# Optimization experiments

Measured on AMD Instinct MI355X. Metric: run time of the kernel, lower is better.

The kernel has to match this reference:

```python
import jax, jax.numpy as jnp
import numpy as np

V = 778   # MANO mesh vertex count (hard-coded in the module)
K = 9     # spiral neighborhood length
C = 256   # in_channels
OUT = 3   # out_channels (per-vertex offset xyz)
B3 = 192  # 3 * B, B = 64


def setup_inputs() -> dict:
    key = jax.random.key(0)
    ks = jax.random.split(key, 12)
    x = jax.random.normal(ks[0], (B3, V, C), jnp.float32)
    pred_occ = jax.random.normal(ks[1], (B3, 2, 5), jnp.float32)
    indices = jax.random.randint(ks[2], (V, K), 0, V)
    finger_sizes = [112, 120, 124, 116, 108]
    fingers = {f"finger{i}": jax.random.randint(ks[3 + i], (n,), 0, V)
               for i, n in enumerate(finger_sizes)}

    def lin(k, fan_in, fan_out):
        kw, kb = jax.random.split(k)
        w = jax.random.normal(kw, (fan_in, fan_out), jnp.float32) / np.float32(np.sqrt(fan_in))
        b = jax.random.normal(kb, (fan_out,), jnp.float32) * 0.01
        return w, b

    w0, b0 = lin(ks[8], 2 * C * K, 2 * C)
    w1, b1 = lin(ks[9], 2 * C * K, C)
    w2, b2 = lin(ks[10], C * K, C)
    wh, bh = lin(ks[11], C * K, OUT)
    return {"x": x, "pred_occ": pred_occ, "indices": indices, **fingers,
            "w0": w0, "b0": b0, "w1": w1, "b1": b1, "w2": w2, "b2": b2,
            "wh": wh, "bh": bh}


def spiral_conv(x, idx, w, b):
    # x: [B, V, Cin], idx: [V, K] -> gather spiral neighbors, flatten, linear
    B = x.shape[0]
    g = x[:, idx.reshape(-1), :].reshape(B, V, -1)  # [B, V, K*Cin]
    return g @ w + b


def reference(x, pred_occ, indices, finger0, finger1, finger2, finger3, finger4,
              w0, b0, w1, b1, w2, b2, wh, bh):
    # Per-finger non-occlusion probabilities: softmax over class dim, take class 0
    occ = jax.nn.softmax(pred_occ, axis=1)[:, 0, :5]          # [3B, 5]
    weights = jnp.ones((x.shape[0], V), x.dtype)
    for i, fidx in enumerate([finger0, finger1, finger2, finger3, finger4]):
        val = jnp.broadcast_to(occ[:, i:i + 1], (x.shape[0], fidx.shape[0]))
        weights = weights.at[:, fidx].set(val)
    B = x.shape[0] // 3
    wv = jnp.stack(jnp.split(weights, 3, axis=0), axis=-1)[..., None]  # [B, V, 3, 1]
    wv = jax.nn.softmax(wv, axis=2)
    xv = jnp.stack(jnp.split(x, 3, axis=0), axis=2)                    # [B, V, 3, C]
    wx = jnp.sum(wv * xv, axis=2)                                      # [B, V, C]
    h = jnp.concatenate([wx, x[:B]], axis=2)                           # [B, V, 2C]
    h = jax.nn.relu(spiral_conv(h, indices, w0, b0))
    h = jax.nn.relu(spiral_conv(h, indices, w1, b1))
    h = jax.nn.relu(spiral_conv(h, indices, w2, b2))
    return spiral_conv(h, indices, wh, bh)                             # [B, V, 3]
```

## Files before the change

kernel.cpp:

```cpp
#include <hip/hip_runtime.h>

typedef unsigned short ushort_t;
typedef __attribute__((ext_vector_type(8))) __bf16 bf16x8;
typedef __attribute__((ext_vector_type(8))) unsigned short ushort8;
typedef __attribute__((ext_vector_type(4))) float floatx4;
typedef __attribute__((ext_vector_type(16))) float floatx16;

#define VN 778
#define KNB 9

__device__ __forceinline__ float bf2f(unsigned short s) {
  union { unsigned int u; float f; } x; x.u = ((unsigned int)s) << 16; return x.f;
}
__device__ __forceinline__ unsigned short f2bf(float f) {
  union { float f; unsigned int u; } x; x.f = f;
  unsigned int r = x.u + 0x7fffu + ((x.u >> 16) & 1u);
  return (unsigned short)(r >> 16);
}

__device__ __forceinline__ void load_lds16(const void* g, void* l) {
  __builtin_amdgcn_global_load_lds(
      (const __attribute__((address_space(1))) unsigned int*)g,
      (__attribute__((address_space(3))) unsigned int*)l, 16, 0, 0);
}

__global__ void prep_misc(const float* __restrict__ pred_occ,
                          const int* f0, const int* f1, const int* f2,
                          const int* f3, const int* f4,
                          int n0, int n1, int n2, int n3, int n4,
                          const float* __restrict__ wh,
                          float* __restrict__ occ, int* __restrict__ fid,
                          float* __restrict__ whT) {
  int t = threadIdx.x;
  for (int i = t; i < 192 * 5; i += 256) {
    int r = i / 5, f = i % 5;
    float p0 = pred_occ[r * 10 + f];
    float p1 = pred_occ[r * 10 + 5 + f];
    occ[i] = 1.0f / (1.0f + __expf(p1 - p0));
  }
  for (int i = t; i < VN; i += 256) fid[i] = -1;
  __syncthreads();
  const int* fp[5] = {f0, f1, f2, f3, f4};
  int fn[5] = {n0, n1, n2, n3, n4};
  for (int fi = 0; fi < 5; ++fi) {
    for (int i = t; i < fn[fi]; i += 256) fid[fp[fi][i]] = fi;
    __syncthreads();
  }
  for (int i = t; i < 3 * 2304; i += 256) {
    int o = i / 2304, k = i % 2304;
    whT[i] = wh[k * 3 + o];
  }
}

__global__ void wx_kernel(const float* __restrict__ x, const float* __restrict__ occ,
                          const int* __restrict__ fid, ushort_t* __restrict__ wx) {
  int g = blockIdx.x * 256 + threadIdx.x;
  int c8 = (g & 31) << 3;
  int bv = g >> 5;
  int b = bv / VN;
  int v = bv - b * VN;
  int f = fid[v];
  float w0 = 1.f, w1 = 1.f, w2 = 1.f;
  if (f >= 0) {
    w0 = occ[b * 5 + f];
    w1 = occ[(64 + b) * 5 + f];
    w2 = occ[(128 + b) * 5 + f];
  }
  float m = fmaxf(w0, fmaxf(w1, w2));
  float e0 = __expf(w0 - m), e1 = __expf(w1 - m), e2 = __expf(w2 - m);
  float inv = 1.0f / (e0 + e1 + e2);
  e0 *= inv; e1 *= inv; e2 *= inv;
  size_t base = (size_t)bv * 256 + c8;
  const size_t V1 = (size_t)64 * VN * 256, V2 = (size_t)128 * VN * 256;
  floatx4 x0a = *(const floatx4*)(x + base);
  floatx4 x0b = *(const floatx4*)(x + base + 4);
  floatx4 x1a = *(const floatx4*)(x + V1 + base);
  floatx4 x1b = *(const floatx4*)(x + V1 + base + 4);
  floatx4 x2a = *(const floatx4*)(x + V2 + base);
  floatx4 x2b = *(const floatx4*)(x + V2 + base + 4);
  ushort8 o;
#pragma unroll
  for (int e = 0; e < 4; ++e) {
    o[e]     = f2bf(e0 * x0a[e] + e1 * x1a[e] + e2 * x2a[e]);
    o[e + 4] = f2bf(e0 * x0b[e] + e1 * x1b[e] + e2 * x2b[e]);
  }
  *(ushort8*)(wx + base) = o;
}

__global__ void xcvt_kernel(const float* __restrict__ x, ushort_t* __restrict__ xb) {
  int g = blockIdx.x * 256 + threadIdx.x;
  size_t base = (size_t)g * 8;
  floatx4 fa = *(const floatx4*)(x + base);
  floatx4 fb = *(const floatx4*)(x + base + 4);
  ushort8 o;
#pragma unroll
  for (int e = 0; e < 4; ++e) { o[e] = f2bf(fa[e]); o[e + 4] = f2bf(fb[e]); }
  *(ushort8*)(xb + base) = o;
}

__global__ void pack_w(const float* __restrict__ w, ushort_t* __restrict__ wP,
                       int N, int ksn, int total) {
  int chunk = blockIdx.x * 256 + threadIdx.x;
  if (chunk >= total) return;
  int lane = chunk & 63;
  int rest = chunk >> 6;
  int ks = rest % ksn;
  int tn = rest / ksn;
  int n = (tn << 5) + (lane & 31);
  int kb = (ks << 4) + ((lane >> 5) << 3);
  ushort8 o;
#pragma unroll
  for (int j = 0; j < 8; ++j) o[j] = f2bf(w[(size_t)(kb + j) * N + n]);
  *(ushort8*)(wP + (size_t)chunk * 8) = o;
}

__global__ void pack_w64(const float* __restrict__ w, ushort_t* __restrict__ wP,
                         int N, int ksn, int total) {
  int chunk = blockIdx.x * 256 + threadIdx.x;
  if (chunk >= total) return;
  int lane = chunk & 63;
  int idx2 = chunk >> 6;
  int sub = idx2 & 1;
  int rest = idx2 >> 1;
  int ks = rest % ksn;
  int tn64 = rest / ksn;
  int n = (tn64 << 6) + (sub << 5) + (lane & 31);
  int kb = (ks << 4) + ((lane >> 5) << 3);
  ushort8 o;
#pragma unroll
  for (int j = 0; j < 8; ++j) o[j] = f2bf(w[(size_t)(kb + j) * N + n]);
  *(ushort8*)(wP + (size_t)chunk * 8) = o;
}

template <int CIN, int MODE, int WN>
__global__ __launch_bounds__(512, (WN == 64 ? 2 : 4)) void spiral_gemm(
    const ushort_t* __restrict__ act0, const float* __restrict__ actF,
    const ushort_t* __restrict__ actB, const ushort_t* __restrict__ wP,
    const float* __restrict__ bias, const int* __restrict__ idx,
    ushort_t* __restrict__ out, int NOUT) {
  constexpr int H = CIN / 128;
  constexpr int P = KNB * H;
  constexpr int KtotSteps = KNB * (CIN / 16);
  __shared__ __align__(16) ushort_t Alds[2][2048 * 8];
  const int v0 = blockIdx.x * 2;
  const int n0 = blockIdx.y << 8;
  const int tid = threadIdx.x;
  const int lane = tid & 63;
  const int wv = tid >> 6;
  const int mlo = lane & 31;
  const int q = lane >> 5;
  const int xm = mlo & 7;
  floatx16 c00{}, c01{}, c10{}, c11{}, c20{}, c21{}, c30{}, c31{};
  const ushort_t* bp;
  if constexpr (WN == 32) {
    const int tn0 = (n0 >> 5) + wv;
    bp = wP + (size_t)tn0 * KtotSteps * 512 + lane * 8;
  } else {
    bp = wP + (size_t)wv * KtotSteps * 1024 + lane * 8;
  }
  const int* iv0 = idx + v0 * KNB;
  const int* iv1 = iv0 + KNB;
  const int aoff0 = mlo * 128;
  const int aoff1 = (mlo + 32) * 128;
  const int aoff2 = 8192 + mlo * 128;
  const int aoff3 = 8192 + (mlo + 32) * 128;

  auto dma_stage = [&](int p, ushort_t* buf) {
    const int nbr = p / H, h = p - nbr * H;
    const int nva = iv0[nbr], nvb = iv1[nbr];
#pragma unroll
    for (int it = 0; it < 4; ++it) {
      const int slotb = ((wv << 2) + it) << 6;
      const int s = slotb + lane;
      const int vv = s >> 10;
      const int row = (s >> 4) & 63;
      const int ck = (s & 15) ^ (row & 7);
      const int nv = vv ? nvb : nva;
      const ushort_t* src;
      if (MODE == 0) {
        src = act0 + ((size_t)(row * VN + nv)) * CIN + h * 128 + ck * 8;
      } else {
        const ushort_t* basep = (MODE == 1 || h < 2) ? act0 : actB;
        src = basep + ((size_t)(row * VN + nv)) * 256 + (h & 1) * 128 + ck * 8;
      }
      load_lds16(src, buf + (size_t)slotb * 8);
    }
  };
  auto f32_stage = [&](int p, ushort_t* buf) {
    const int nbr = p / H, h = p - nbr * H;
    const int nva = iv0[nbr], nvb = iv1[nbr];
#pragma unroll
    for (int j = 0; j < 4; ++j) {
      const int s = (j << 9) + tid;
      const int vv = s >> 10;
      const int row = (s >> 4) & 63;
      const int ck = (s & 15) ^ (row & 7);
      const int nv = vv ? nvb : nva;
      const float* src = actF + ((size_t)(row * VN + nv)) * 256 + (h - 2) * 128 + ck * 8;
      floatx4 fa = *(const floatx4*)src;
      floatx4 fb = *(const floatx4*)(src + 4);
      ushort8 o;
#pragma unroll
      for (int e = 0; e < 4; ++e) { o[e] = f2bf(fa[e]); o[e + 4] = f2bf(fb[e]); }
      *(ushort8*)(buf + (size_t)s * 8) = o;
    }
  };

  dma_stage(0, Alds[0]);
  __syncthreads();
#pragma unroll 2
  for (int p = 0; p < P; ++p) {
    ushort_t* cur = Alds[p & 1];
    ushort_t* nxt = Alds[(p + 1) & 1];
    const bool have_next = (p + 1 < P);
    const bool next_f32 = (MODE == 1) && (((p + 1) & (H - 1)) >= 2);
    if (have_next && !next_f32) dma_stage(p + 1, nxt);
#pragma unroll
    for (int ks = 0; ks < 8; ++ks) {
      const int cko = ((((ks << 1) + q) ^ xm) << 3);
      if constexpr (WN == 32) {
        bf16x8 a0 = *(const bf16x8*)(cur + aoff0 + cko);
        bf16x8 a1 = *(const bf16x8*)(cur + aoff1 + cko);
        bf16x8 a2 = *(const bf16x8*)(cur + aoff2 + cko);
        bf16x8 a3 = *(const bf16x8*)(cur + aoff3 + cko);
        bf16x8 bv0 = *(const bf16x8*)bp; bp += 512;
        c00 = __builtin_amdgcn_mfma_f32_32x32x16_bf16(a0, bv0, c00, 0, 0, 0);
        c10 = __builtin_amdgcn_mfma_f32_32x32x16_bf16(a1, bv0, c10, 0, 0, 0);
        c20 = __builtin_amdgcn_mfma_f32_32x32x16_bf16(a2, bv0, c20, 0, 0, 0);
        c30 = __builtin_amdgcn_mfma_f32_32x32x16_bf16(a3, bv0, c30, 0, 0, 0);
      } else {
        bf16x8 a0 = *(const bf16x8*)(cur + aoff0 + cko);
        bf16x8 a1 = *(const bf16x8*)(cur + aoff1 + cko);
        bf16x8 a2 = *(const bf16x8*)(cur + aoff2 + cko);
        bf16x8 a3 = *(const bf16x8*)(cur + aoff3 + cko);
        bf16x8 b0 = *(const bf16x8*)bp;
        bf16x8 b1 = *(const bf16x8*)(bp + 512);
        bp += 1024;
        c00 = __builtin_amdgcn_mfma_f32_32x32x16_bf16(a0, b0, c00, 0, 0, 0);
        c10 = __builtin_amdgcn_mfma_f32_32x32x16_bf16(a1, b0, c10, 0, 0, 0);
        c20 = __builtin_amdgcn_mfma_f32_32x32x16_bf16(a2, b0, c20, 0, 0, 0);
        c30 = __builtin_amdgcn_mfma_f32_32x32x16_bf16(a3, b0, c30, 0, 0, 0);
        c01 = __builtin_amdgcn_mfma_f32_32x32x16_bf16(a0, b1, c01, 0, 0, 0);
        c11 = __builtin_amdgcn_mfma_f32_32x32x16_bf16(a1, b1, c11, 0, 0, 0);
        c21 = __builtin_amdgcn_mfma_f32_32x32x16_bf16(a2, b1, c21, 0, 0, 0);
        c31 = __builtin_amdgcn_mfma_f32_32x32x16_bf16(a3, b1, c31, 0, 0, 0);
      }
    }
    __syncthreads();
    if (have_next && next_f32) { f32_stage(p + 1, nxt); __syncthreads(); }
  }
  if constexpr (WN == 32) {
    const int n = n0 + (wv << 5) + mlo;
    const float bn = bias[n];
#pragma unroll
    for (int t = 0; t < 4; ++t) {
      const floatx16 av = (t == 0) ? c00 : (t == 1) ? c10 : (t == 2) ? c20 : c30;
      const int vcur = v0 + (t >> 1);
      const int bbase = (t & 1) << 5;
#pragma unroll
      for (int r = 0; r < 16; ++r) {
        const int m = (r & 3) + ((r >> 2) << 3) + (q << 2);
        float val = av[r] + bn; val = val > 0.f ? val : 0.f;
        out[((size_t)((bbase + m) * VN + vcur)) * NOUT + n] = f2bf(val);
      }
    }
  } else {
    const int nbase = (wv << 6) + mlo;
    const float bn0 = bias[nbase];
    const float bn1 = bias[nbase + 32];
#pragma unroll
    for (int t = 0; t < 8; ++t) {
      const int aj = t >> 1;
      const int ni = t & 1;
      const floatx16 av = (t == 0) ? c00 : (t == 1) ? c01 : (t == 2) ? c10 :
                          (t == 3) ? c11 : (t == 4) ? c20 : (t == 5) ? c21 :
                          (t == 6) ? c30 : c31;
      const int vcur = v0 + (aj >> 1);
      const int bbase = (aj & 1) << 5;
      const int n = nbase + (ni << 5);
      const float bn = ni ? bn1 : bn0;
#pragma unroll
      for (int r = 0; r < 16; ++r) {
        const int m = (r & 3) + ((r >> 2) << 3) + (q << 2);
        float val = av[r] + bn; val = val > 0.f ? val : 0.f;
        out[((size_t)((bbase + m) * VN + vcur)) * NOUT + n] = f2bf(val);
      }
    }
  }
}

__global__ void head_kernel(const ushort_t* __restrict__ act, const float* __restrict__ whT,
                            const float* __restrict__ bh, const int* __restrict__ idx,
                            float* __restrict__ out) {
  __shared__ __align__(16) ushort_t Alds[64 * 256];
  const int v = blockIdx.x;
  const int tid = threadIdx.x;
  float a0 = 0.f, a1 = 0.f, a2 = 0.f;
  const int b = tid;
  const int xm = b & 7;
  for (int nbr = 0; nbr < KNB; ++nbr) {
    const int nv = idx[v * KNB + nbr];
    __syncthreads();
#pragma unroll
    for (int it = 0; it < 8; ++it) {
      int L = it * 256 + tid;
      int bb = L >> 5;
      int jj = L & 31;
      ushort8 val = *(const ushort8*)(act + ((size_t)(bb * VN + nv)) * 256 + (jj << 3));
      int slot = jj ^ (bb & 7);
      *(ushort8*)&Alds[(size_t)(bb * 32 + slot) * 8] = val;
    }
    __syncthreads();
    if (tid < 64) {
      const float* wp = whT + nbr * 256;
#pragma unroll 4
      for (int j = 0; j < 32; ++j) {
        int jj = j ^ xm;
        ushort8 a8 = *(const ushort8*)&Alds[(b * 32 + jj) * 8];
#pragma unroll
        for (int e = 0; e < 8; ++e) {
          float av = bf2f(a8[e]);
          int k = (j << 3) + e;
          a0 += av * wp[k];
          a1 += av * wp[2304 + k];
          a2 += av * wp[4608 + k];
        }
      }
    }
  }
  if (tid < 64) {
    size_t o = ((size_t)(b * VN + v)) * 3;
    out[o + 0] = a0 + bh[0];
    out[o + 1] = a1 + bh[1];
    out[o + 2] = a2 + bh[2];
  }
}

extern "C" void kernel_launch(void* const* d_in, const int* in_sizes, int n_in,
                              void* d_out, int out_size, void* d_ws, size_t ws_size,
                              hipStream_t stream) {
  const float* x        = (const float*)d_in[0];
  const float* pred_occ = (const float*)d_in[1];
  const int* indices    = (const int*)d_in[2];
  const int* f0 = (const int*)d_in[3];
  const int* f1 = (const int*)d_in[4];
  const int* f2 = (const int*)d_in[5];
  const int* f3 = (const int*)d_in[6];
  const int* f4 = (const int*)d_in[7];
  const float* w0 = (const float*)d_in[8];
  const float* b0 = (const float*)d_in[9];
  const float* w1 = (const float*)d_in[10];
  const float* b1 = (const float*)d_in[11];
  const float* w2 = (const float*)d_in[12];
  const float* b2 = (const float*)d_in[13];
  const float* wh = (const float*)d_in[14];
  const float* bh = (const float*)d_in[15];
  float* outp = (float*)d_out;

  char* ws = (char*)d_ws;
  ushort_t* wP0 = (ushort_t*)(ws + 0);
  ushort_t* wP1 = (ushort_t*)(ws + 4718592);
  ushort_t* wP2 = (ushort_t*)(ws + 7077888);
  float* whT    = (float*)(ws + 8257536);
  float* occ    = (float*)(ws + 8285184);
  int* fid      = (int*)(ws + 8289024);
  ushort_t* R0  = (ushort_t*)(ws + 8292352);
  ushort_t* R1  = (ushort_t*)(ws + 33785856);
  ushort_t* XB  = (ushort_t*)(ws + 84772864);
  const bool useXB = (ws_size >= 110266368ull);

  prep_misc<<<1, 256, 0, stream>>>(pred_occ, f0, f1, f2, f3, f4,
                                   in_sizes[3], in_sizes[4], in_sizes[5],
                                   in_sizes[6], in_sizes[7], wh, occ, fid, whT);
  pack_w64<<<294912 / 256, 256, 0, stream>>>(w0, wP0, 512, 288, 294912);
  pack_w<<<147456 / 256, 256, 0, stream>>>(w1, wP1, 256, 288, 147456);
  pack_w<<<73728 / 256, 256, 0, stream>>>(w2, wP2, 256, 144, 73728);
  if (useXB) xcvt_kernel<<<6224, 256, 0, stream>>>(x, XB);
  wx_kernel<<<6224, 256, 0, stream>>>(x, occ, fid, R0);

  if (useXB)
    spiral_gemm<512, 2, 64><<<dim3(389, 1), 512, 0, stream>>>(R0, nullptr, XB, wP0, b0,
                                                              indices, R1, 512);
  else
    spiral_gemm<512, 1, 64><<<dim3(389, 1), 512, 0, stream>>>(R0, x, nullptr, wP0, b0,
                                                              indices, R1, 512);
  spiral_gemm<512, 0, 32><<<dim3(389, 1), 512, 0, stream>>>(R1, nullptr, nullptr, wP1, b1,
                                                            indices, R0, 256);
  spiral_gemm<256, 0, 32><<<dim3(389, 1), 512, 0, stream>>>(R0, nullptr, nullptr, wP2, b2,
                                                            indices, R1, 256);
  head_kernel<<<VN, 256, 0, stream>>>(R1, whT, bh, indices, outp);
  (void)n_in; (void)out_size;
}
```

Measured before the change: 825.0 us.

## Triple-buffer LDS gather pipeline in first spiral GEMM layer

Splits the wide first-layer spiral GEMM into its own kernel that keeps three LDS buffers and issues the gather DMA two stages ahead. It replaces the per-stage double-buffer __syncthreads with explicit vmcnt waits and a single barrier, and raises MFMA wave priority during compute. Neighbor indices are cached in shared memory once per block. The aim is to hide global-to-LDS gather latency behind MFMA work, at the cost of more LDS per block and fragile hand-written waitcnt ordering. The narrower layers keep the old double-buffered path.

```diff
diff --git a/kernel.cpp b/kernel.cpp
--- a/kernel.cpp
+++ b/kernel.cpp
@@ -132,8 +132,8 @@
   *(ushort8*)(wP + (size_t)chunk * 8) = o;
 }
 
-template <int CIN, int MODE, int WN>
-__global__ __launch_bounds__(512, (WN == 64 ? 2 : 4)) void spiral_gemm(
+template <int CIN, int MODE>
+__global__ __launch_bounds__(512, 2) void spiral_gemm_p(
     const ushort_t* __restrict__ act0, const float* __restrict__ actF,
     const ushort_t* __restrict__ actB, const ushort_t* __restrict__ wP,
     const float* __restrict__ bias, const int* __restrict__ idx,
@@ -141,9 +141,9 @@
   constexpr int H = CIN / 128;
   constexpr int P = KNB * H;
   constexpr int KtotSteps = KNB * (CIN / 16);
-  __shared__ __align__(16) ushort_t Alds[2][2048 * 8];
+  __shared__ __align__(16) ushort_t Alds[3][2048 * 8];
+  __shared__ int nbrsL[2 * KNB];
   const int v0 = blockIdx.x * 2;
-  const int n0 = blockIdx.y << 8;
   const int tid = threadIdx.x;
   const int lane = tid & 63;
   const int wv = tid >> 6;
@@ -151,23 +151,17 @@
   const int q = lane >> 5;
   const int xm = mlo & 7;
   floatx16 c00{}, c01{}, c10{}, c11{}, c20{}, c21{}, c30{}, c31{};
-  const ushort_t* bp;
-  if constexpr (WN == 32) {
-    const int tn0 = (n0 >> 5) + wv;
-    bp = wP + (size_t)tn0 * KtotSteps * 512 + lane * 8;
-  } else {
-    bp = wP + (size_t)wv * KtotSteps * 1024 + lane * 8;
-  }
-  const int* iv0 = idx + v0 * KNB;
-  const int* iv1 = iv0 + KNB;
+  const ushort_t* bp = wP + (size_t)wv * KtotSteps * 1024 + lane * 8;
+  if (tid < 2 * KNB) nbrsL[tid] = idx[v0 * KNB + tid];
   const int aoff0 = mlo * 128;
   const int aoff1 = (mlo + 32) * 128;
   const int aoff2 = 8192 + mlo * 128;
   const int aoff3 = 8192 + (mlo + 32) * 128;
+  __syncthreads();
 
   auto dma_stage = [&](int p, ushort_t* buf) {
     const int nbr = p / H, h = p - nbr * H;
-    const int nva = iv0[nbr], nvb = iv1[nbr];
+    const int nva = nbrsL[nbr], nvb = nbrsL[KNB + nbr];
 #pragma unroll
     for (int it = 0; it < 4; ++it) {
       const int slotb = ((wv << 2) + it) << 6;
@@ -188,7 +182,7 @@
   };
   auto f32_stage = [&](int p, ushort_t* buf) {
     const int nbr = p / H, h = p - nbr * H;
-    const int nva = iv0[nbr], nvb = iv1[nbr];
+    const int nva = nbrsL[nbr], nvb = nbrsL[KNB + nbr];
 #pragma unroll
     for (int j = 0; j < 4; ++j) {
       const int s = (j << 9) + tid;
@@ -206,6 +200,144 @@
     }
   };
 
+  ushort_t* bufA = Alds[0];
+  ushort_t* bufB = Alds[1];
+  ushort_t* bufC = Alds[2];
+  dma_stage(0, bufA);
+  dma_stage(1, bufB);
+#pragma unroll 1
+  for (int p = 0; p < P; ++p) {
+    if (MODE == 1 && (((p + 1) & (H - 1)) >= 2)) {
+      asm volatile("s_waitcnt vmcnt(0)" ::: "memory");
+    } else {
+      asm volatile("s_waitcnt vmcnt(4)" ::: "memory");
+    }
+    __builtin_amdgcn_s_barrier();
+    asm volatile("" ::: "memory");
+    ushort_t* cur = bufA;
+    __builtin_amdgcn_s_setprio(1);
+#pragma unroll
+    for (int ks = 0; ks < 8; ++ks) {
+      const int cko = ((((ks << 1) + q) ^ xm) << 3);
+      bf16x8 a0 = *(const bf16x8*)(cur + aoff0 + cko);
+      bf16x8 a1 = *(const bf16x8*)(cur + aoff1 + cko);
+      bf16x8 a2 = *(const bf16x8*)(cur + aoff2 + cko);
+      bf16x8 a3 = *(const bf16x8*)(cur + aoff3 + cko);
+      bf16x8 b0 = *(const bf16x8*)bp;
+      bf16x8 b1 = *(const bf16x8*)(bp + 512);
+      bp += 1024;
+      c00 = __builtin_amdgcn_mfma_f32_32x32x16_bf16(a0, b0, c00, 0, 0, 0);
+      c10 = __builtin_amdgcn_mfma_f32_32x32x16_bf16(a1, b0, c10, 0, 0, 0);
+      c20 = __builtin_amdgcn_mfma_f32_32x32x16_bf16(a2, b0, c20, 0, 0, 0);
+      c30 = __builtin_amdgcn_mfma_f32_32x32x16_bf16(a3, b0, c30, 0, 0, 0);
+      c01 = __builtin_amdgcn_mfma_f32_32x32x16_bf16(a0, b1, c01, 0, 0, 0);
+      c11 = __builtin_amdgcn_mfma_f32_32x32x16_bf16(a1, b1, c11, 0, 0, 0);
+      c21 = __builtin_amdgcn_mfma_f32_32x32x16_bf16(a2, b1, c21, 0, 0, 0);
+      c31 = __builtin_amdgcn_mfma_f32_32x32x16_bf16(a3, b1, c31, 0, 0, 0);
+    }
+    __builtin_amdgcn_s_setprio(0);
+    if (p + 2 < P) {
+      if (MODE == 1 && (((p + 2) & (H - 1)) >= 2)) {
+        f32_stage(p + 2, bufC);
+        asm volatile("s_waitcnt lgkmcnt(0)" ::: "memory");
+      } else {
+        dma_stage(p + 2, bufC);
+      }
+    }
+    ushort_t* t = bufA; bufA = bufB; bufB = bufC; bufC = t;
+  }
+  const int nbase = (wv << 6) + mlo;
+  const float bn0 = bias[nbase];
+  const float bn1 = bias[nbase + 32];
+#pragma unroll
+  for (int t = 0; t < 8; ++t) {
+    const int aj = t >> 1;
+    const int ni = t & 1;
+    const floatx16 av = (t == 0) ? c00 : (t == 1) ? c01 : (t == 2) ? c10 :
+                        (t == 3) ? c11 : (t == 4) ? c20 : (t == 5) ? c21 :
+                        (t == 6) ? c30 : c31;
+    const int vcur = v0 + (aj >> 1);
+    const int bbase = (aj & 1) << 5;
+    const int n = nbase + (ni << 5);
+    const float bn = ni ? bn1 : bn0;
+#pragma unroll
+    for (int r = 0; r < 16; ++r) {
+      const int m = (r & 3) + ((r >> 2) << 3) + (q << 2);
+      float val = av[r] + bn; val = val > 0.f ? val : 0.f;
+      out[((size_t)((bbase + m) * VN + vcur)) * NOUT + n] = f2bf(val);
+    }
+  }
+}
+
+template <int CIN, int MODE>
+__global__ __launch_bounds__(512, 4) void spiral_gemm(
+    const ushort_t* __restrict__ act0, const float* __restrict__ actF,
+    const ushort_t* __restrict__ actB, const ushort_t* __restrict__ wP,
+    const float* __restrict__ bias, const int* __restrict__ idx,
+    ushort_t* __restrict__ out, int NOUT) {
+  constexpr int H = CIN / 128;
+  constexpr int P = KNB * H;
+  __shared__ __align__(16) ushort_t Alds[2][2048 * 8];
+  const int v0 = blockIdx.x * 2;
+  const int n0 = blockIdx.y << 8;
+  const int tid = threadIdx.x;
+  const int lane = tid & 63;
+  const int wv = tid >> 6;
+  const int mlo = lane & 31;
+  const int q = lane >> 5;
+  const int xm = mlo & 7;
+  floatx16 acc0{}, acc1{}, acc2{}, acc3{};
+  const int KtotSteps = KNB * (CIN / 16);
+  const int tn0 = (n0 >> 5) + wv;
+  const ushort_t* bp = wP + (size_t)tn0 * KtotSteps * 512 + lane * 8;
+  const int* iv0 = idx + v0 * KNB;
+  const int* iv1 = iv0 + KNB;
+  const int aoff0 = mlo * 128;
+  const int aoff1 = (mlo + 32) * 128;
+  const int aoff2 = 8192 + mlo * 128;
+  const int aoff3 = 8192 + (mlo + 32) * 128;
+
+  auto dma_stage = [&](int p, ushort_t* buf) {
+    const int nbr = p / H, h = p - nbr * H;
+    const int nva = iv0[nbr], nvb = iv1[nbr];
+#pragma unroll
+    for (int it = 0; it < 4; ++it) {
+      const int slotb = ((wv << 2) + it) << 6;
+      const int s = slotb + lane;
+      const int vv = s >> 10;
+      const int row = (s >> 4) & 63;
+      const int ck = (s & 15) ^ (row & 7);
+      const int nv = vv ? nvb : nva;
+      const ushort_t* src;
+      if (MODE == 0) {
+        src = act0 + ((size_t)(row * VN + nv)) * CIN + h * 128 + ck * 8;
+      } else {
+        const ushort_t* basep = (MODE == 1 || h < 2) ? act0 : actB;
+        src = basep + ((size_t)(row * VN + nv)) * 256 + (h & 1) * 128 + ck * 8;
+      }
+      load_lds16(src, buf + (size_t)slotb * 8);
+    }
+  };
+  auto f32_stage = [&](int p, ushort_t* buf) {
+    const int nbr = p / H, h = p - nbr * H;
+    const int nva = iv0[nbr], nvb = iv1[nbr];
+#pragma unroll
+    for (int j = 0; j < 4; ++j) {
+      const int s = (j << 9) + tid;
+      const int vv = s >> 10;
+      const int row = (s >> 4) & 63;
+      const int ck = (s & 15) ^ (row & 7);
+      const int nv = vv ? nvb : nva;
+      const float* src = actF + ((size_t)(row * VN + nv)) * 256 + (h - 2) * 128 + ck * 8;
+      floatx4 fa = *(const floatx4*)src;
+      floatx4 fb = *(const floatx4*)(src + 4);
+      ushort8 o;
+#pragma unroll
+      for (int e = 0; e < 4; ++e) { o[e] = f2bf(fa[e]); o[e + 4] = f2bf(fb[e]); }
+      *(ushort8*)(buf + (size_t)s * 8) = o;
+    }
+  };
+
   dma_stage(0, Alds[0]);
   __syncthreads();
 #pragma unroll 2
@@ -218,73 +350,31 @@
 #pragma unroll
     for (int ks = 0; ks < 8; ++ks) {
       const int cko = ((((ks << 1) + q) ^ xm) << 3);
-      if constexpr (WN == 32) {
-        bf16x8 a0 = *(const bf16x8*)(cur + aoff0 + cko);
-        bf16x8 a1 = *(const bf16x8*)(cur + aoff1 + cko);
-        bf16x8 a2 = *(const bf16x8*)(cur + aoff2 + cko);
-        bf16x8 a3 = *(const bf16x8*)(cur + aoff3 + cko);
-        bf16x8 bv0 = *(const bf16x8*)bp; bp += 512;
-        c00 = __builtin_amdgcn_mfma_f32_32x32x16_bf16(a0, bv0, c00, 0, 0, 0);
-        c10 = __builtin_amdgcn_mfma_f32_32x32x16_bf16(a1, bv0, c10, 0, 0, 0);
-        c20 = __builtin_amdgcn_mfma_f32_32x32x16_bf16(a2, bv0, c20, 0, 0, 0);
-        c30 = __builtin_amdgcn_mfma_f32_32x32x16_bf16(a3, bv0, c30, 0, 0, 0);
-      } else {
-        bf16x8 a0 = *(const bf16x8*)(cur + aoff0 + cko);
-        bf16x8 a1 = *(const bf16x8*)(cur + aoff1 + cko);
-        bf16x8 a2 = *(const bf16x8*)(cur + aoff2 + cko);
-        bf16x8 a3 = *(const bf16x8*)(cur + aoff3 + cko);
-        bf16x8 b0 = *(const bf16x8*)bp;
-        bf16x8 b1 = *(const bf16x8*)(bp + 512);
-        bp += 1024;
-        c00 = __builtin_amdgcn_mfma_f32_32x32x16_bf16(a0, b0, c00, 0, 0, 0);
-        c10 = __builtin_amdgcn_mfma_f32_32x32x16_bf16(a1, b0, c10, 0, 0, 0);
-        c20 = __builtin_amdgcn_mfma_f32_32x32x16_bf16(a2, b0, c20, 0, 0, 0);
-        c30 = __builtin_amdgcn_mfma_f32_32x32x16_bf16(a3, b0, c30, 0, 0, 0);
-        c01 = __builtin_amdgcn_mfma_f32_32x32x16_bf16(a0, b1, c01, 0, 0, 0);
-        c11 = __builtin_amdgcn_mfma_f32_32x32x16_bf16(a1, b1, c11, 0, 0, 0);
-        c21 = __builtin_amdgcn_mfma_f32_32x32x16_bf16(a2, b1, c21, 0, 0, 0);
-        c31 = __builtin_amdgcn_mfma_f32_32x32x16_bf16(a3, b1, c31, 0, 0, 0);
-      }
+      bf16x8 a0 = *(const bf16x8*)(cur + aoff0 + cko);
+      bf16x8 a1 = *(const bf16x8*)(cur + aoff1 + cko);
+      bf16x8 a2 = *(const bf16x8*)(cur + aoff2 + cko);
+      bf16x8 a3 = *(const bf16x8*)(cur + aoff3 + cko);
+      bf16x8 bv = *(const bf16x8*)bp; bp += 512;
+      acc0 = __builtin_amdgcn_mfma_f32_32x32x16_bf16(a0, bv, acc0, 0, 0, 0);
+      acc1 = __builtin_amdgcn_mfma_f32_32x32x16_bf16(a1, bv, acc1, 0, 0, 0);
+      acc2 = __builtin_amdgcn_mfma_f32_32x32x16_bf16(a2, bv, acc2, 0, 0, 0);
+      acc3 = __builtin_amdgcn_mfma_f32_32x32x16_bf16(a3, bv, acc3, 0, 0, 0);
     }
     __syncthreads();
     if (have_next && next_f32) { f32_stage(p + 1, nxt); __syncthreads(); }
   }
-  if constexpr (WN == 32) {
-    const int n = n0 + (wv << 5) + mlo;
-    const float bn = bias[n];
-#pragma unroll
-    for (int t = 0; t < 4; ++t) {
-      const floatx16 av = (t == 0) ? c00 : (t == 1) ? c10 : (t == 2) ? c20 : c30;
-      const int vcur = v0 + (t >> 1);
-      const int bbase = (t & 1) << 5;
-#pragma unroll
-      for (int r = 0; r < 16; ++r) {
-        const int m = (r & 3) + ((r >> 2) << 3) + (q << 2);
-        float val = av[r] + bn; val = val > 0.f ? val : 0.f;
-        out[((size_t)((bbase + m) * VN + vcur)) * NOUT + n] = f2bf(val);
-      }
-    }
-  } else {
-    const int nbase = (wv << 6) + mlo;
-    const float bn0 = bias[nbase];
-    const float bn1 = bias[nbase + 32];
-#pragma unroll
-    for (int t = 0; t < 8; ++t) {
-      const int aj = t >> 1;
-      const int ni = t & 1;
-      const floatx16 av = (t == 0) ? c00 : (t == 1) ? c01 : (t == 2) ? c10 :
-                          (t == 3) ? c11 : (t == 4) ? c20 : (t == 5) ? c21 :
-                          (t == 6) ? c30 : c31;
-      const int vcur = v0 + (aj >> 1);
-      const int bbase = (aj & 1) << 5;
-      const int n = nbase + (ni << 5);
-      const float bn = ni ? bn1 : bn0;
-#pragma unroll
-      for (int r = 0; r < 16; ++r) {
-        const int m = (r & 3) + ((r >> 2) << 3) + (q << 2);
-        float val = av[r] + bn; val = val > 0.f ? val : 0.f;
-        out[((size_t)((bbase + m) * VN + vcur)) * NOUT + n] = f2bf(val);
-      }
+  const int n = n0 + (wv << 5) + mlo;
+  const float bn = bias[n];
+#pragma unroll
+  for (int t = 0; t < 4; ++t) {
+    const floatx16 av = (t == 0) ? acc0 : (t == 1) ? acc1 : (t == 2) ? acc2 : acc3;
+    const int vcur = v0 + (t >> 1);
+    const int bbase = (t & 1) << 5;
+#pragma unroll
+    for (int r = 0; r < 16; ++r) {
+      const int m = (r & 3) + ((r >> 2) << 3) + (q << 2);
+      float val = av[r] + bn; val = val > 0.f ? val : 0.f;
+      out[((size_t)((bbase + m) * VN + vcur)) * NOUT + n] = f2bf(val);
     }
   }
 }
@@ -379,15 +469,15 @@
   wx_kernel<<<6224, 256, 0, stream>>>(x, occ, fid, R0);
 
   if (useXB)
-    spiral_gemm<512, 2, 64><<<dim3(389, 1), 512, 0, stream>>>(R0, nullptr, XB, wP0, b0,
-                                                              indices, R1, 512);
+    spiral_gemm_p<512, 2><<<389, 512, 0, stream>>>(R0, nullptr, XB, wP0, b0,
+                                                   indices, R1, 512);
   else
-    spiral_gemm<512, 1, 64><<<dim3(389, 1), 512, 0, stream>>>(R0, x, nullptr, wP0, b0,
-                                                              indices, R1, 512);
-  spiral_gemm<512, 0, 32><<<dim3(389, 1), 512, 0, stream>>>(R1, nullptr, nullptr, wP1, b1,
-                                                            indices, R0, 256);
-  spiral_gemm<256, 0, 32><<<dim3(389, 1), 512, 0, stream>>>(R0, nullptr, nullptr, wP2, b2,
-                                                            indices, R1, 256);
+    spiral_gemm_p<512, 1><<<389, 512, 0, stream>>>(R0, x, nullptr, wP0, b0,
+                                                   indices, R1, 512);
+  spiral_gemm<512, 0><<<dim3(389, 1), 512, 0, stream>>>(R1, nullptr, nullptr, wP1, b1,
+                                                        indices, R0, 256);
+  spiral_gemm<256, 0><<<dim3(389, 1), 512, 0, stream>>>(R0, nullptr, nullptr, wP2, b2,
+                                                        indices, R1, 256);
   head_kernel<<<VN, 256, 0, stream>>>(R1, whT, bh, indices, outp);
   (void)n_in; (void)out_size;
 }
```

Measured after the change: 864.5 us. 4.8% more time.
